# Performance work log

Measured on AMD Instinct MI355X. Metric: run time of the kernel, lower is better.

The kernel has to match this reference:

```python
import jax, jax.numpy as jnp
import numpy as np

MARGIN = 0.3
EPS = 1e-6  # torch pairwise_distance eps (added to the difference before norm)


def _sample_triplets(labels, B):
    """Vectorized equivalent of the per-row nonzero()+randint() mining loop.

    pos_idx[i] ~ Uniform{j : labels[j] == labels[i]}   (always non-empty: i itself)
    neg_idx[i] ~ Uniform{j : labels[j] != labels[i]}, fallback Uniform[0,B) if empty.
    Uniform-noise argmax over the masked set == uniform random choice.
    """
    key = jax.random.key(42)
    k1, k2, k3 = jax.random.split(key, 3)
    eq = labels[:, None] == labels[None, :]              # [B, B]
    pos_idx = jnp.argmax(jnp.where(eq, jax.random.uniform(k1, (B, B)), -1.0), axis=1)
    neg_scores = jnp.where(~eq, jax.random.uniform(k2, (B, B)), -1.0)
    has_neg = jnp.any(~eq, axis=1)
    neg_idx = jnp.where(has_neg,
                        jnp.argmax(neg_scores, axis=1),
                        jax.random.randint(k3, (B,), 0, B))
    return pos_idx, neg_idx


def _pdist(X, A, D):
    """out[i, j] = || A[j] - X[i] + EPS ||_2  (torch pairwise_distance semantics),
    computed via gram matrices instead of a [B,B,D] intermediate:
    ||a - x + eps||^2 = ||a||^2 + ||x||^2 - 2 a.x + 2*eps*(sum a - sum x) + D*eps^2.
    """
    sq = (jnp.sum(A * A, axis=1)[None, :]
          + jnp.sum(X * X, axis=1)[:, None]
          - 2.0 * (X @ A.T)
          + 2.0 * EPS * (jnp.sum(A, axis=1)[None, :] - jnp.sum(X, axis=1)[:, None])
          + D * EPS * EPS)
    return jnp.sqrt(jnp.maximum(sq, 1e-12))


def setup_inputs() -> dict:
    key = jax.random.key(0)
    kf, kl = jax.random.split(key)
    B, D, NUM_IDS = 4096, 1024, 512
    features = jax.random.normal(kf, (B, D), dtype=jnp.float32)
    labels = jax.random.randint(kl, (B,), 0, NUM_IDS, dtype=jnp.int32)
    return {"features": features, "labels": labels}


def reference(features, labels):
    B, D = features.shape
    pos_idx, neg_idx = _sample_triplets(labels, B)
    P = features[pos_idx]   # positives, [B, D]
    N = features[neg_idx]   # negatives, [B, D]
    # Original torch code stacks positives/negatives as [B,1,D] vs anchors [B,D],
    # so TripletMarginLoss broadcasts to ALL-PAIRS [B,B] distances:
    # dap[i, j] = ||anchor_j - positive_i + eps||, same for dan.
    dap = _pdist(P, features, D)  # [B, B]
    dan = _pdist(N, features, D)  # [B, B]
    return jnp.mean(jax.nn.relu(dap - dan + MARGIN))
```

## Files before the change

kernel.cpp:

```cpp
#include <hip/hip_runtime.h>
#include <stdint.h>

#define BSZ 4096
#define DIM 1024
#define EPSV 1e-6f
#define MARGINV 0.3f
#define SROWS 4
#define SAMPLE_BLOCKS (BSZ / SROWS)
#define PREP_BLOCKS (BSZ / 4)

#define TF_ROT(x0, x1, r) { x0 += x1; x1 = ((x1 << r) | (x1 >> (32 - r))); x1 ^= x0; }

__host__ __device__ __forceinline__ void threefry2x32(uint32_t k0, uint32_t k1,
                                                      uint32_t c0, uint32_t c1,
                                                      uint32_t& o0, uint32_t& o1) {
  uint32_t ks2 = k0 ^ k1 ^ 0x1BD11BDAu;
  uint32_t x0 = c0 + k0;
  uint32_t x1 = c1 + k1;
  TF_ROT(x0, x1, 13) TF_ROT(x0, x1, 15) TF_ROT(x0, x1, 26) TF_ROT(x0, x1, 6)
  x0 += k1;  x1 += ks2 + 1u;
  TF_ROT(x0, x1, 17) TF_ROT(x0, x1, 29) TF_ROT(x0, x1, 16) TF_ROT(x0, x1, 24)
  x0 += ks2; x1 += k0 + 2u;
  TF_ROT(x0, x1, 13) TF_ROT(x0, x1, 15) TF_ROT(x0, x1, 26) TF_ROT(x0, x1, 6)
  x0 += k0;  x1 += k1 + 3u;
  TF_ROT(x0, x1, 17) TF_ROT(x0, x1, 29) TF_ROT(x0, x1, 16) TF_ROT(x0, x1, 24)
  x0 += k1;  x1 += ks2 + 4u;
  TF_ROT(x0, x1, 13) TF_ROT(x0, x1, 15) TF_ROT(x0, x1, 26) TF_ROT(x0, x1, 6)
  x0 += ks2; x1 += k0 + 5u;
  o0 = x0; o1 = x1;
}

#define TFR2(r) { xa0 += xa1; xb0 += xb1; \
                  xa1 = ((xa1 << r) | (xa1 >> (32 - r))) ^ xa0; \
                  xb1 = ((xb1 << r) | (xb1 >> (32 - r))) ^ xb0; }

__device__ __forceinline__ void threefry_x2(uint32_t k0, uint32_t k1,
                                            uint32_t ca, uint32_t cb,
                                            uint32_t& oa, uint32_t& ob) {
  const uint32_t ks2 = k0 ^ k1 ^ 0x1BD11BDAu;
  uint32_t xa0 = k0, xa1 = ca + k1;
  uint32_t xb0 = k0, xb1 = cb + k1;
  TFR2(13) TFR2(15) TFR2(26) TFR2(6)
  xa0 += k1;  xa1 += ks2 + 1u;  xb0 += k1;  xb1 += ks2 + 1u;
  TFR2(17) TFR2(29) TFR2(16) TFR2(24)
  xa0 += ks2; xa1 += k0 + 2u;   xb0 += ks2; xb1 += k0 + 2u;
  TFR2(13) TFR2(15) TFR2(26) TFR2(6)
  xa0 += k0;  xa1 += k1 + 3u;   xb0 += k0;  xb1 += k1 + 3u;
  TFR2(17) TFR2(29) TFR2(16) TFR2(24)
  xa0 += k1;  xa1 += ks2 + 4u;  xb0 += k1;  xb1 += ks2 + 4u;
  TFR2(13) TFR2(15) TFR2(26) TFR2(6)
  xa0 += ks2; xa1 += k0 + 5u;   xb0 += ks2; xb1 += k0 + 5u;
  oa = xa0 ^ xa1;
  ob = xb0 ^ xb1;
}

__device__ __forceinline__ uint16_t f2bf(float f) {
  uint32_t u = __float_as_uint(f);
  u += 0x7FFFu + ((u >> 16) & 1u);
  return (uint16_t)(u >> 16);
}

__global__ __launch_bounds__(256, 4) void prep_sample_kernel(
    const float* __restrict__ F, uint8_t* __restrict__ Fq,
    float* __restrict__ norm2, float* __restrict__ sums, float* __restrict__ nv,
    const int* __restrict__ labels, int* __restrict__ pos_idx, int* __restrict__ neg_idx,
    uint32_t p0, uint32_t p1, uint32_t n0, uint32_t n1) {
  const int t = threadIdx.x;
  if (blockIdx.x >= SAMPLE_BLOCKS) {
    const int w = t >> 6, l = t & 63;
    const int r = (blockIdx.x - SAMPLE_BLOCKS) * 4 + w;
    const float4* src = (const float4*)(F + (size_t)r * DIM);
    uint32_t* dst = (uint32_t*)(Fq + (size_t)r * DIM);
    float s = 0.f, q = 0.f;
#pragma unroll
    for (int c = 0; c < 4; ++c) {
      float4 v = src[c * 64 + l];
      s += (v.x + v.y) + (v.z + v.w);
      q += v.x * v.x + v.y * v.y + v.z * v.z + v.w * v.w;
      int wd = 0;
      wd = __builtin_amdgcn_cvt_pk_fp8_f32(v.x, v.y, wd, false);
      wd = __builtin_amdgcn_cvt_pk_fp8_f32(v.z, v.w, wd, true);
      dst[c * 64 + l] = (uint32_t)wd;
    }
    for (int off = 32; off; off >>= 1) { s += __shfl_xor(s, off); q += __shfl_xor(q, off); }
    if (l == 0) {
      norm2[r] = q; sums[r] = s;
      nv[r] = q + 2.0f * EPSV * s;
    }
    return;
  }
  __shared__ int plist[SROWS][64];
  __shared__ int pcnt[SROWS];
  __shared__ unsigned long long swp[SROWS];
  __shared__ unsigned long long swn[SROWS];
  const int i0 = blockIdx.x * SROWS;
  if (t < SROWS) { pcnt[t] = 0; swp[t] = 0ull; swn[t] = 0ull; }
  int lj[16];
#pragma unroll
  for (int c = 0; c < 16; ++c) lj[c] = labels[c * 256 + t];
  __syncthreads();
  const int lane = t & 63;
#pragma unroll 1
  for (int r = 0; r < SROWS; ++r) {
    const int li = labels[i0 + r];
    const uint32_t base = (uint32_t)(i0 + r) * (uint32_t)BSZ + (uint32_t)t;
    uint32_t bestn = 0u;
#pragma unroll
    for (int c = 0; c < 16; c += 2) {
      uint32_t bitsA, bitsB;
      threefry_x2(n0, n1, base + (uint32_t)(c * 256), base + (uint32_t)((c + 1) * 256),
                  bitsA, bitsB);
      const uint32_t packA = ((bitsA >> 5) & 0xFFFFFFF0u) | (uint32_t)(15 - c);
      const uint32_t packB = ((bitsB >> 5) & 0xFFFFFFF0u) | (uint32_t)(14 - c);
      const uint32_t vA = (lj[c] == li) ? 0u : packA;
      const uint32_t vB = (lj[c + 1] == li) ? 0u : packB;
      const uint32_t m = vA > vB ? vA : vB;
      if (m > bestn) bestn = m;
    }
    unsigned long long keyn = 0ull;
    if (bestn) {
      const int c = 15 - (int)(bestn & 15u);
      const int j = c * 256 + t;
      keyn = ((unsigned long long)(bestn >> 4) << 32) | (uint32_t)(~j);
    }
    for (int off = 32; off; off >>= 1) {
      unsigned long long o = __shfl_xor(keyn, off);
      if (o > keyn) keyn = o;
    }
    if (lane == 0) atomicMax(&swn[r], keyn);
#pragma unroll
    for (int c = 0; c < 16; ++c) {
      if (lj[c] == li) {
        int sl = atomicAdd(&pcnt[r], 1);
        if (sl < 64) plist[r][sl] = c * 256 + t;
      }
    }
  }
  __syncthreads();
  const int w = t >> 6;
  {
    const int cnt = pcnt[w] < 64 ? pcnt[w] : 64;
    if (lane < cnt) {
      const int j = plist[w][lane];
      uint32_t y0, y1;
      threefry2x32(p0, p1, 0u, (uint32_t)(i0 + w) * (uint32_t)BSZ + (uint32_t)j, y0, y1);
      const unsigned long long key =
          ((unsigned long long)((y0 ^ y1) >> 9) << 32) | (uint32_t)(~j);
      atomicMax(&swp[w], key);
    }
  }
  __syncthreads();
  if (t < SROWS) {
    pos_idx[i0 + t] = (int)(~(uint32_t)swp[t]);
    const unsigned long long vn = swn[t];
    neg_idx[i0 + t] = (vn == 0ull) ? 0 : (int)(~(uint32_t)vn);
  }
}

using int8v = __attribute__((ext_vector_type(8))) int;
using int4v = __attribute__((ext_vector_type(4))) int;
using f32x4 = __attribute__((ext_vector_type(4))) float;

__device__ __forceinline__ void async_load16(const void* g, void* l) {
  __builtin_amdgcn_global_load_lds((__attribute__((address_space(1))) void*)g,
                                   (__attribute__((address_space(3))) void*)l, 16, 0, 0);
}

__global__ __launch_bounds__(256) void gemm_kernel(const uint8_t* __restrict__ Fq,
                                                   uint16_t* __restrict__ Gb) {
  const int p = blockIdx.x;
  int by = (int)((sqrtf(8.0f * (float)p + 1.0f) - 1.0f) * 0.5f);
  if ((by + 1) * (by + 2) / 2 <= p) ++by;
  if (by * (by + 1) / 2 > p) --by;
  const int bx = p - by * (by + 1) / 2;

  __shared__ __align__(16) uint8_t lA[128 * 128];
  __shared__ __align__(16) uint8_t lB[128 * 128];
  const int t = threadIdx.x;
  const int l = t & 63;
  const int w = t >> 6;
  const int wm = (w >> 1) * 64;
  const int wn = (w & 1) * 64;
  const int bm = bx * 128;
  const int bn = by * 128;

  f32x4 acc[4][4] = {};

  const int srow = t >> 3;
  const int scol = (((t & 7) ^ ((t >> 3) & 7)) << 4);
  const uint8_t* gA0 = Fq + (size_t)(bm + srow) * DIM + scol;
  const uint8_t* gB0 = Fq + (size_t)(bn + srow) * DIM + scol;

  const int fr = l & 15;
  const int c0 = (l >> 4) * 2;
  int offA[4][2], offB[4][2];
#pragma unroll
  for (int tm = 0; tm < 4; ++tm) {
    const int fra = wm + tm * 16 + fr, sw = fra & 7;
    offA[tm][0] = fra * 128 + ((c0 ^ sw) << 4);
    offA[tm][1] = fra * 128 + (((c0 + 1) ^ sw) << 4);
    const int frb = wn + tm * 16 + fr, sb = frb & 7;
    offB[tm][0] = frb * 128 + ((c0 ^ sb) << 4);
    offB[tm][1] = frb * 128 + (((c0 + 1) ^ sb) << 4);
  }

  for (int it = 0; it < 8; ++it) {
    const int k0 = it * 128;
    __syncthreads();
#pragma unroll
    for (int ld = 0; ld < 4; ++ld) {
      async_load16(gA0 + (size_t)ld * 32 * DIM + k0, (char*)lA + (ld * 256 + t) * 16);
      async_load16(gB0 + (size_t)ld * 32 * DIM + k0, (char*)lB + (ld * 256 + t) * 16);
    }
    __syncthreads();
    int8v av[4], bv[4];
#pragma unroll
    for (int tm = 0; tm < 4; ++tm) {
      int4v alo = *(const int4v*)&lA[offA[tm][0]];
      int4v ahi = *(const int4v*)&lA[offA[tm][1]];
      av[tm] = __builtin_shufflevector(alo, ahi, 0, 1, 2, 3, 4, 5, 6, 7);
      int4v blo = *(const int4v*)&lB[offB[tm][0]];
      int4v bhi = *(const int4v*)&lB[offB[tm][1]];
      bv[tm] = __builtin_shufflevector(blo, bhi, 0, 1, 2, 3, 4, 5, 6, 7);
    }
#pragma unroll
    for (int tm = 0; tm < 4; ++tm)
#pragma unroll
      for (int tn = 0; tn < 4; ++tn)
        acc[tm][tn] = __builtin_amdgcn_mfma_scale_f32_16x16x128_f8f6f4(
            av[tm], bv[tn], acc[tm][tn],
            0, 0,
            0, 0x7F7F7F7F,
            0, 0x7F7F7F7F);
  }
  const int cr = (l >> 4) * 4;
  const int cc = l & 15;
#pragma unroll
  for (int tm = 0; tm < 4; ++tm)
#pragma unroll
    for (int tn = 0; tn < 4; ++tn) {
      const int row0 = bm + wm + tm * 16 + cr;
      const int col  = bn + wn + tn * 16 + cc;
      ushort h0 = f2bf(acc[tm][tn][0]), h1 = f2bf(acc[tm][tn][1]);
      ushort h2 = f2bf(acc[tm][tn][2]), h3 = f2bf(acc[tm][tn][3]);
      Gb[(size_t)(row0 + 0) * BSZ + col] = h0;
      Gb[(size_t)(row0 + 1) * BSZ + col] = h1;
      Gb[(size_t)(row0 + 2) * BSZ + col] = h2;
      Gb[(size_t)(row0 + 3) * BSZ + col] = h3;
      ushort4 v = make_ushort4(h0, h1, h2, h3);
      *(ushort4*)&Gb[(size_t)col * BSZ + row0] = v;
    }
}

__device__ __forceinline__ float bfl(uint32_t w) { return __uint_as_float(w << 16); }
__device__ __forceinline__ float bfh(uint32_t w) { return __uint_as_float(w & 0xFFFF0000u); }

__global__ __launch_bounds__(256) void loss_kernel(const uint16_t* __restrict__ Gb,
                                                   const float* __restrict__ norm2,
                                                   const float* __restrict__ sums,
                                                   const float* __restrict__ nv,
                                                   const int* __restrict__ pos_idx,
                                                   const int* __restrict__ neg_idx,
                                                   float* __restrict__ partial) {
  const int i = blockIdx.x, t = threadIdx.x;
  const int a = pos_idx[i], b = neg_idx[i];
  const float deps2 = (float)DIM * EPSV * EPSV;
  const float ca = norm2[a] - 2.0f * EPSV * sums[a] + deps2;
  const float cb = norm2[b] - 2.0f * EPSV * sums[b] + deps2;
  const uint4* Ga = (const uint4*)(Gb + (size_t)a * BSZ);
  const uint4* Gn = (const uint4*)(Gb + (size_t)b * BSZ);
  const float4* N4 = (const float4*)nv;
  uint4 ga[2], gn[2];
  float4 njv[4];
  ga[0] = Ga[t * 2]; ga[1] = Ga[t * 2 + 1];
  gn[0] = Gn[t * 2]; gn[1] = Gn[t * 2 + 1];
#pragma unroll
  for (int k = 0; k < 4; ++k) njv[k] = N4[t * 4 + k];
  float s = 0.f;
#pragma unroll
  for (int h = 0; h < 2; ++h) {
    const uint4 gau = ga[h], gnu = gn[h];
    float gav[8] = {bfl(gau.x), bfh(gau.x), bfl(gau.y), bfh(gau.y),
                    bfl(gau.z), bfh(gau.z), bfl(gau.w), bfh(gau.w)};
    float gnv[8] = {bfl(gnu.x), bfh(gnu.x), bfl(gnu.y), bfh(gnu.y),
                    bfl(gnu.z), bfh(gnu.z), bfl(gnu.w), bfh(gnu.w)};
    const float4 na = njv[h * 2], nb = njv[h * 2 + 1];
    float nj[8] = {na.x, na.y, na.z, na.w, nb.x, nb.y, nb.z, nb.w};
#pragma unroll
    for (int e = 0; e < 8; ++e) {
      const float dap = sqrtf(fmaxf(fmaf(-2.f, gav[e], nj[e] + ca), 1e-12f));
      const float dan = sqrtf(fmaxf(fmaf(-2.f, gnv[e], nj[e] + cb), 1e-12f));
      s += fmaxf(dap - dan + MARGINV, 0.f);
    }
  }
  for (int off = 32; off; off >>= 1) s += __shfl_xor(s, off);
  __shared__ float ps[4];
  const int w = t >> 6, lane = t & 63;
  if (lane == 0) ps[w] = s;
  __syncthreads();
  if (t == 0) partial[i] = (ps[0] + ps[1]) + (ps[2] + ps[3]);
}

__global__ __launch_bounds__(256) void finalize_kernel(const float* __restrict__ partial,
                                                       float* __restrict__ out) {
  const int t = threadIdx.x;
  const float4* P4 = (const float4*)partial;
  float s = 0.f;
#pragma unroll
  for (int k = 0; k < 4; ++k) {
    float4 v = P4[k * 256 + t];
    s += (v.x + v.y) + (v.z + v.w);
  }
  for (int off = 32; off; off >>= 1) s += __shfl_xor(s, off);
  __shared__ float ps[4];
  const int w = t >> 6, lane = t & 63;
  if (lane == 0) ps[w] = s;
  __syncthreads();
  if (t == 0)
    out[0] = ((ps[0] + ps[1]) + (ps[2] + ps[3])) * (1.0f / ((float)BSZ * (float)BSZ));
}

extern "C" void kernel_launch(void* const* d_in, const int* in_sizes, int n_in,
                              void* d_out, int out_size, void* d_ws, size_t ws_size,
                              hipStream_t stream) {
  const float* feat = (const float*)d_in[0];
  const int* labels = (const int*)d_in[1];
  float* out = (float*)d_out;

  char* ws = (char*)d_ws;
  uint16_t* Gb     = (uint16_t*)ws;
  uint8_t* Fq      = (uint8_t*)(ws + (size_t)33554432);
  float* norm2     = (float*)(ws + (size_t)37748736);
  float* sums      = (float*)(ws + (size_t)37748736 + 16384);
  float* nv        = (float*)(ws + (size_t)37748736 + 32768);
  int* pos_idx     = (int*)  (ws + (size_t)37748736 + 49152);
  int* neg_idx     = (int*)  (ws + (size_t)37748736 + 65536);
  float* partial   = (float*)(ws + (size_t)37748736 + 81920);

  uint32_t k1a, k1b, k2a, k2b;
  threefry2x32(0u, 42u, 0u, 0u, k1a, k1b);
  threefry2x32(0u, 42u, 0u, 1u, k2a, k2b);

  prep_sample_kernel<<<dim3(SAMPLE_BLOCKS + PREP_BLOCKS), dim3(256), 0, stream>>>(
      feat, Fq, norm2, sums, nv, labels, pos_idx, neg_idx, k1a, k1b, k2a, k2b);
  gemm_kernel<<<dim3(528), dim3(256), 0, stream>>>(Fq, Gb);
  loss_kernel<<<dim3(BSZ), dim3(256), 0, stream>>>(Gb, norm2, sums, nv, pos_idx,
                                                   neg_idx, partial);
  finalize_kernel<<<dim3(1), dim3(256), 0, stream>>>(partial, out);
}
```

Baseline: 143.1 us.

## Move triplet sampling blocks from prep kernel into GEMM kernel launch

The RNG-heavy triplet sampling blocks are moved out of the prep kernel and appended as extra blocks to the GEMM launch, reusing the GEMM's shared-memory buffers for their scratch arrays. The prep kernel becomes a pure quantize/norm pass. The aim is to let the compute-bound sampling run alongside the 528-block GEMM, which alone underfills the GPU, so sampling is no longer on the critical path before the GEMM. The risk is that the GEMM now carries launch_bounds(256,4), which could constrain its registers, and that sampling blocks may contend with GEMM tiles.

Measured after the change: 137.8 us, median of 2. -3.7%, faster.

```diff
diff --git a/kernel.cpp b/kernel.cpp
--- a/kernel.cpp
+++ b/kernel.cpp
@@ -6,8 +6,8 @@
 #define EPSV 1e-6f
 #define MARGINV 0.3f
 #define SROWS 4
+#define GEMM_BLOCKS 528
 #define SAMPLE_BLOCKS (BSZ / SROWS)
-#define PREP_BLOCKS (BSZ / 4)
 
 #define TF_ROT(x0, x1, r) { x0 += x1; x1 = ((x1 << r) | (x1 >> (32 - r))); x1 ^= x0; }
 
@@ -60,100 +60,30 @@
   return (uint16_t)(u >> 16);
 }
 
-__global__ __launch_bounds__(256, 4) void prep_sample_kernel(
-    const float* __restrict__ F, uint8_t* __restrict__ Fq,
-    float* __restrict__ norm2, float* __restrict__ sums, float* __restrict__ nv,
-    const int* __restrict__ labels, int* __restrict__ pos_idx, int* __restrict__ neg_idx,
-    uint32_t p0, uint32_t p1, uint32_t n0, uint32_t n1) {
-  const int t = threadIdx.x;
-  if (blockIdx.x >= SAMPLE_BLOCKS) {
-    const int w = t >> 6, l = t & 63;
-    const int r = (blockIdx.x - SAMPLE_BLOCKS) * 4 + w;
-    const float4* src = (const float4*)(F + (size_t)r * DIM);
-    uint32_t* dst = (uint32_t*)(Fq + (size_t)r * DIM);
-    float s = 0.f, q = 0.f;
-#pragma unroll
-    for (int c = 0; c < 4; ++c) {
-      float4 v = src[c * 64 + l];
-      s += (v.x + v.y) + (v.z + v.w);
-      q += v.x * v.x + v.y * v.y + v.z * v.z + v.w * v.w;
-      int wd = 0;
-      wd = __builtin_amdgcn_cvt_pk_fp8_f32(v.x, v.y, wd, false);
-      wd = __builtin_amdgcn_cvt_pk_fp8_f32(v.z, v.w, wd, true);
-      dst[c * 64 + l] = (uint32_t)wd;
-    }
-    for (int off = 32; off; off >>= 1) { s += __shfl_xor(s, off); q += __shfl_xor(q, off); }
-    if (l == 0) {
-      norm2[r] = q; sums[r] = s;
-      nv[r] = q + 2.0f * EPSV * s;
-    }
-    return;
-  }
-  __shared__ int plist[SROWS][64];
-  __shared__ int pcnt[SROWS];
-  __shared__ unsigned long long swp[SROWS];
-  __shared__ unsigned long long swn[SROWS];
-  const int i0 = blockIdx.x * SROWS;
-  if (t < SROWS) { pcnt[t] = 0; swp[t] = 0ull; swn[t] = 0ull; }
-  int lj[16];
-#pragma unroll
-  for (int c = 0; c < 16; ++c) lj[c] = labels[c * 256 + t];
-  __syncthreads();
-  const int lane = t & 63;
-#pragma unroll 1
-  for (int r = 0; r < SROWS; ++r) {
-    const int li = labels[i0 + r];
-    const uint32_t base = (uint32_t)(i0 + r) * (uint32_t)BSZ + (uint32_t)t;
-    uint32_t bestn = 0u;
-#pragma unroll
-    for (int c = 0; c < 16; c += 2) {
-      uint32_t bitsA, bitsB;
-      threefry_x2(n0, n1, base + (uint32_t)(c * 256), base + (uint32_t)((c + 1) * 256),
-                  bitsA, bitsB);
-      const uint32_t packA = ((bitsA >> 5) & 0xFFFFFFF0u) | (uint32_t)(15 - c);
-      const uint32_t packB = ((bitsB >> 5) & 0xFFFFFFF0u) | (uint32_t)(14 - c);
-      const uint32_t vA = (lj[c] == li) ? 0u : packA;
-      const uint32_t vB = (lj[c + 1] == li) ? 0u : packB;
-      const uint32_t m = vA > vB ? vA : vB;
-      if (m > bestn) bestn = m;
-    }
-    unsigned long long keyn = 0ull;
-    if (bestn) {
-      const int c = 15 - (int)(bestn & 15u);
-      const int j = c * 256 + t;
-      keyn = ((unsigned long long)(bestn >> 4) << 32) | (uint32_t)(~j);
-    }
-    for (int off = 32; off; off >>= 1) {
-      unsigned long long o = __shfl_xor(keyn, off);
-      if (o > keyn) keyn = o;
-    }
-    if (lane == 0) atomicMax(&swn[r], keyn);
-#pragma unroll
-    for (int c = 0; c < 16; ++c) {
-      if (lj[c] == li) {
-        int sl = atomicAdd(&pcnt[r], 1);
-        if (sl < 64) plist[r][sl] = c * 256 + t;
-      }
-    }
-  }
-  __syncthreads();
-  const int w = t >> 6;
-  {
-    const int cnt = pcnt[w] < 64 ? pcnt[w] : 64;
-    if (lane < cnt) {
-      const int j = plist[w][lane];
-      uint32_t y0, y1;
-      threefry2x32(p0, p1, 0u, (uint32_t)(i0 + w) * (uint32_t)BSZ + (uint32_t)j, y0, y1);
-      const unsigned long long key =
-          ((unsigned long long)((y0 ^ y1) >> 9) << 32) | (uint32_t)(~j);
-      atomicMax(&swp[w], key);
-    }
-  }
-  __syncthreads();
-  if (t < SROWS) {
-    pos_idx[i0 + t] = (int)(~(uint32_t)swp[t]);
-    const unsigned long long vn = swn[t];
-    neg_idx[i0 + t] = (vn == 0ull) ? 0 : (int)(~(uint32_t)vn);
+__global__ __launch_bounds__(256) void prep_kernel(const float* __restrict__ F,
+                                                   uint8_t* __restrict__ Fq,
+                                                   float* __restrict__ norm2,
+                                                   float* __restrict__ sums,
+                                                   float* __restrict__ nv) {
+  const int w = threadIdx.x >> 6, l = threadIdx.x & 63;
+  const int r = blockIdx.x * 4 + w;
+  const float4* src = (const float4*)(F + (size_t)r * DIM);
+  uint32_t* dst = (uint32_t*)(Fq + (size_t)r * DIM);
+  float s = 0.f, q = 0.f;
+#pragma unroll
+  for (int c = 0; c < 4; ++c) {
+    float4 v = src[c * 64 + l];
+    s += (v.x + v.y) + (v.z + v.w);
+    q += v.x * v.x + v.y * v.y + v.z * v.z + v.w * v.w;
+    int wd = 0;
+    wd = __builtin_amdgcn_cvt_pk_fp8_f32(v.x, v.y, wd, false);
+    wd = __builtin_amdgcn_cvt_pk_fp8_f32(v.z, v.w, wd, true);
+    dst[c * 64 + l] = (uint32_t)wd;
+  }
+  for (int off = 32; off; off >>= 1) { s += __shfl_xor(s, off); q += __shfl_xor(q, off); }
+  if (l == 0) {
+    norm2[r] = q; sums[r] = s;
+    nv[r] = q + 2.0f * EPSV * s;
   }
 }
 
@@ -166,17 +96,90 @@
                                    (__attribute__((address_space(3))) void*)l, 16, 0, 0);
 }
 
-__global__ __launch_bounds__(256) void gemm_kernel(const uint8_t* __restrict__ Fq,
-                                                   uint16_t* __restrict__ Gb) {
+__global__ __launch_bounds__(256, 4) void gemm_sample_kernel(
+    const uint8_t* __restrict__ Fq, uint16_t* __restrict__ Gb,
+    const int* __restrict__ labels, int* __restrict__ pos_idx, int* __restrict__ neg_idx,
+    uint32_t p0, uint32_t p1, uint32_t n0, uint32_t n1) {
+  __shared__ __align__(16) uint8_t lA[128 * 128];
+  __shared__ __align__(16) uint8_t lB[128 * 128];
+  const int t = threadIdx.x;
+
+  if (blockIdx.x >= GEMM_BLOCKS) {
+    int* plist = (int*)lA;
+    int* pcnt = (int*)(lA + SROWS * 64 * 4);
+    unsigned long long* swp = (unsigned long long*)(lB);
+    unsigned long long* swn = (unsigned long long*)(lB + 64);
+    const int i0 = (blockIdx.x - GEMM_BLOCKS) * SROWS;
+    if (t < SROWS) { pcnt[t] = 0; swp[t] = 0ull; swn[t] = 0ull; }
+    int lj[16];
+#pragma unroll
+    for (int c = 0; c < 16; ++c) lj[c] = labels[c * 256 + t];
+    __syncthreads();
+    const int lane = t & 63;
+#pragma unroll 1
+    for (int r = 0; r < SROWS; ++r) {
+      const int li = labels[i0 + r];
+      const uint32_t base = (uint32_t)(i0 + r) * (uint32_t)BSZ + (uint32_t)t;
+      uint32_t bestn = 0u;
+#pragma unroll
+      for (int c = 0; c < 16; c += 2) {
+        uint32_t bitsA, bitsB;
+        threefry_x2(n0, n1, base + (uint32_t)(c * 256), base + (uint32_t)((c + 1) * 256),
+                    bitsA, bitsB);
+        const uint32_t packA = ((bitsA >> 5) & 0xFFFFFFF0u) | (uint32_t)(15 - c);
+        const uint32_t packB = ((bitsB >> 5) & 0xFFFFFFF0u) | (uint32_t)(14 - c);
+        const uint32_t vA = (lj[c] == li) ? 0u : packA;
+        const uint32_t vB = (lj[c + 1] == li) ? 0u : packB;
+        const uint32_t m = vA > vB ? vA : vB;
+        if (m > bestn) bestn = m;
+      }
+      unsigned long long keyn = 0ull;
+      if (bestn) {
+        const int c = 15 - (int)(bestn & 15u);
+        const int j = c * 256 + t;
+        keyn = ((unsigned long long)(bestn >> 4) << 32) | (uint32_t)(~j);
+      }
+      for (int off = 32; off; off >>= 1) {
+        unsigned long long o = __shfl_xor(keyn, off);
+        if (o > keyn) keyn = o;
+      }
+      if (lane == 0) atomicMax(&swn[r], keyn);
+#pragma unroll
+      for (int c = 0; c < 16; ++c) {
+        if (lj[c] == li) {
+          int sl = atomicAdd(&pcnt[r], 1);
+          if (sl < 64) plist[r * 64 + sl] = c * 256 + t;
+        }
+      }
+    }
+    __syncthreads();
+    const int w = t >> 6;
+    {
+      const int cnt = pcnt[w] < 64 ? pcnt[w] : 64;
+      if (lane < cnt) {
+        const int j = plist[w * 64 + lane];
+        uint32_t y0, y1;
+        threefry2x32(p0, p1, 0u, (uint32_t)(i0 + w) * (uint32_t)BSZ + (uint32_t)j, y0, y1);
+        const unsigned long long key =
+            ((unsigned long long)((y0 ^ y1) >> 9) << 32) | (uint32_t)(~j);
+        atomicMax(&swp[w], key);
+      }
+    }
+    __syncthreads();
+    if (t < SROWS) {
+      pos_idx[i0 + t] = (int)(~(uint32_t)swp[t]);
+      const unsigned long long vn = swn[t];
+      neg_idx[i0 + t] = (vn == 0ull) ? 0 : (int)(~(uint32_t)vn);
+    }
+    return;
+  }
+
   const int p = blockIdx.x;
   int by = (int)((sqrtf(8.0f * (float)p + 1.0f) - 1.0f) * 0.5f);
   if ((by + 1) * (by + 2) / 2 <= p) ++by;
   if (by * (by + 1) / 2 > p) --by;
   const int bx = p - by * (by + 1) / 2;
 
-  __shared__ __align__(16) uint8_t lA[128 * 128];
-  __shared__ __align__(16) uint8_t lB[128 * 128];
-  const int t = threadIdx.x;
   const int l = t & 63;
   const int w = t >> 6;
   const int wm = (w >> 1) * 64;
@@ -341,9 +344,9 @@
   threefry2x32(0u, 42u, 0u, 0u, k1a, k1b);
   threefry2x32(0u, 42u, 0u, 1u, k2a, k2b);
 
-  prep_sample_kernel<<<dim3(SAMPLE_BLOCKS + PREP_BLOCKS), dim3(256), 0, stream>>>(
-      feat, Fq, norm2, sums, nv, labels, pos_idx, neg_idx, k1a, k1b, k2a, k2b);
-  gemm_kernel<<<dim3(528), dim3(256), 0, stream>>>(Fq, Gb);
+  prep_kernel<<<dim3(BSZ / 4), dim3(256), 0, stream>>>(feat, Fq, norm2, sums, nv);
+  gemm_sample_kernel<<<dim3(GEMM_BLOCKS + SAMPLE_BLOCKS), dim3(256), 0, stream>>>(
+      Fq, Gb, labels, pos_idx, neg_idx, k1a, k1b, k2a, k2b);
   loss_kernel<<<dim3(BSZ), dim3(256), 0, stream>>>(Gb, norm2, sums, nv, pos_idx,
                                                    neg_idx, partial);
   finalize_kernel<<<dim3(1), dim3(256), 0, stream>>>(partial, out);
```
